# Kernel tuning notes

Hardware: AMD Instinct MI355X
Metric: run time of the kernel (lower is better)

Reference implementation:

```python
import jax, jax.numpy as jnp
import numpy as np

B, L, D, RATIO = 256, 197, 768, 8
DK = D // RATIO  # 96


def _mk_linear(key, out_f, in_f):
    kw, kb = jax.random.split(key)
    W = jax.random.normal(kw, (out_f, in_f), jnp.float32) * 0.02  # xavier_normal gain=0.02 scale
    b = jax.random.normal(kb, (out_f,), jnp.float32) * 0.02
    return W, b


def setup_inputs() -> dict:
    key = jax.random.key(0)
    ks = jax.random.split(key, 10)
    x = jax.random.normal(ks[0], (B, L, D), jnp.float32)
    y = jax.random.normal(ks[1], (B, L, D), jnp.float32)
    Wk1, bk1 = _mk_linear(ks[2], DK, D)
    Wk2, bk2 = _mk_linear(ks[3], DK, D)
    Wks, bks = _mk_linear(ks[4], DK, DK)
    Wl1, bl1 = _mk_linear(ks[5], L, L)
    Wl2, bl2 = _mk_linear(ks[6], L, L)
    Wv1, bv1 = _mk_linear(ks[7], D, D)
    Wv2, bv2 = _mk_linear(ks[8], D, D)
    # torch inits gammas to 0; use small nonzero values so outputs/grads are non-trivial
    g = jax.random.normal(ks[9], (2,), jnp.float32) * 0.1
    gamma1 = g[:1]
    gamma2 = g[1:]
    return dict(x=x, y=y, Wk1=Wk1, bk1=bk1, Wk2=Wk2, bk2=bk2, Wks=Wks, bks=bks,
                Wl1=Wl1, bl1=bl1, Wl2=Wl2, bl2=bl2, Wv1=Wv1, bv1=bv1,
                Wv2=Wv2, bv2=bv2, gamma1=gamma1, gamma2=gamma2)


def reference(x, y, Wk1, bk1, Wk2, bk2, Wks, bks, Wl1, bl1, Wl2, bl2,
              Wv1, bv1, Wv2, bv2, gamma1, gamma2):
    b, l, d = x.shape
    # shared-projected keys (B, L, DK)
    k1 = (x @ Wk1.T + bk1) @ Wks.T + bks
    k2 = (y @ Wk2.T + bk2) @ Wks.T + bks
    # faithful to torch: .view(B, -1, L) is a raw reshape (scrambles layout), then permute
    k1r = k1.reshape(b, -1, l).swapaxes(1, 2)   # (B, L, DK)
    k2r = k2.reshape(b, -1, l)                  # (B, DK, L)
    energy = jnp.einsum('blc,bcm->blm', k1r, k2r)  # (B, L, L)
    att1 = jax.nn.softmax(energy @ Wl1.T + bl1, axis=-1)                   # att_y_on_x
    att2 = jax.nn.softmax(energy.swapaxes(1, 2) @ Wl2.T + bl2, axis=-1)    # att_x_on_y
    v2 = y @ Wv2.T + bv2  # (B, L, D)
    out_y_on_x = jnp.einsum('bdl,blm->bdm', v2.swapaxes(1, 2), att1).reshape(b, l, d)
    out_x = gamma1 * out_y_on_x + x
    v1 = x @ Wv1.T + bv1
    out_x_on_y = jnp.einsum('bdl,blm->bdm', v1.swapaxes(1, 2), att2).reshape(b, l, d)
    out_y = gamma2 * out_x_on_y + y
    return (out_x, out_y)
```

## Files before the change

kernel.cpp:

```cpp
#include <hip/hip_runtime.h>
#include <math.h>

typedef unsigned short ushort;
typedef __attribute__((ext_vector_type(4))) unsigned short bfx4;
typedef __attribute__((ext_vector_type(8))) short short8;
typedef __attribute__((ext_vector_type(8))) unsigned short ushort8;
typedef __attribute__((ext_vector_type(4))) float f32x4;
typedef unsigned int u32;

#define VM_WAIT(N) asm volatile("s_waitcnt vmcnt(" #N ")" ::: "memory")
#define SBAR() asm volatile("s_barrier" ::: "memory")

__device__ __forceinline__ int swz4(int row) {
  return (row & 3) ^ ((row >> 2) & 3);
}

__device__ __forceinline__ ushort f2bf(float f) {
  u32 u = __float_as_uint(f);
  return (ushort)((u + 0x7FFF + ((u >> 16) & 1)) >> 16);
}
__device__ __forceinline__ float bf2f(ushort u) {
  u32 v = ((u32)u) << 16;
  return __uint_as_float(v);
}

__device__ __forceinline__ void gload16(const void* g, void* l) {
  __builtin_amdgcn_global_load_lds(
      (const __attribute__((address_space(1))) u32*)g,
      (__attribute__((address_space(3))) u32*)l, 16, 0, 0);
}

#define BKK 32
#define LDSP 68
__global__ __launch_bounds__(256) void gemm_generic(
    const float* __restrict__ A, const float* __restrict__ Bm, const float* __restrict__ Bm2,
    float* __restrict__ C, float* __restrict__ C2,
    int M, int N, int K, long sAi, long sAk, long sBj, long sBk, long sCi)
{
  __shared__ __align__(16) float lds_a[BKK * LDSP];
  __shared__ __align__(16) float lds_b[BKK * LDSP];
  const float* Bb = blockIdx.z ? Bm2 : Bm;
  float* Cc = blockIdx.z ? C2 : C;
  const int i0 = blockIdx.y * 64;
  const int j0 = blockIdx.x * 64;
  const int tid = threadIdx.x;
  const int tx = tid & 15, ty = tid >> 4;
  float acc[4][4] = {};
  for (int k0 = 0; k0 < K; k0 += BKK) {
    for (int idx = tid; idx < BKK * 64; idx += 256) {
      int kk = idx & (BKK - 1), ii = idx >> 5;
      int gi = i0 + ii, gk = k0 + kk;
      lds_a[kk * LDSP + ii] = (gi < M && gk < K) ? A[(long)gi * sAi + (long)gk * sAk] : 0.f;
    }
    for (int idx = tid; idx < BKK * 64; idx += 256) {
      int kk = idx & (BKK - 1), jj = idx >> 5;
      int gj = j0 + jj, gk = k0 + kk;
      lds_b[kk * LDSP + jj] = (gj < N && gk < K) ? Bb[(long)gj * sBj + (long)gk * sBk] : 0.f;
    }
    __syncthreads();
    #pragma unroll
    for (int kk = 0; kk < BKK; ++kk) {
      const float4 a4 = *reinterpret_cast<const float4*>(&lds_a[kk * LDSP + ty * 4]);
      const float4 b4 = *reinterpret_cast<const float4*>(&lds_b[kk * LDSP + tx * 4]);
      const float av[4] = {a4.x, a4.y, a4.z, a4.w};
      const float bv[4] = {b4.x, b4.y, b4.z, b4.w};
      #pragma unroll
      for (int a = 0; a < 4; ++a)
        #pragma unroll
        for (int b = 0; b < 4; ++b)
          acc[a][b] = fmaf(av[a], bv[b], acc[a][b]);
    }
    __syncthreads();
  }
  for (int a = 0; a < 4; ++a) {
    int gi = i0 + ty * 4 + a;
    if (gi >= M) continue;
    for (int b = 0; b < 4; ++b) {
      int gj = j0 + tx * 4 + b;
      if (gj >= N) continue;
      Cc[(long)gi * sCi + gj] = acc[a][b];
    }
  }
}

__global__ __launch_bounds__(256) void mfma_gemm(
    const ushort* __restrict__ A0, const ushort* __restrict__ A1,
    const ushort* __restrict__ B0, const ushort* __restrict__ B1,
    const float* __restrict__ bias0, const float* __restrict__ bias1,
    ushort* __restrict__ C0, ushort* __restrict__ C1,
    int M, int N, int K, long sAi, long sBj, long sCi)
{
  __shared__ ushort As[128 * 64];
  __shared__ ushort Bs[128 * 64];
  const int which = blockIdx.z;
  const ushort* Ab = which ? A1 : A0;
  const ushort* Bb = which ? B1 : B0;
  const float* bias = which ? bias1 : bias0;
  ushort* C = which ? C1 : C0;
  const int i0 = blockIdx.y * 128;
  const int j0 = blockIdx.x * 128;
  const int tid = threadIdx.x;
  const int wave = tid >> 6, lane = tid & 63;
  const int wm = wave >> 1, wn = wave & 1;
  const int col16 = lane & 15, krow = lane >> 4;

  f32x4 acc[4][4] = {};

  for (int k0 = 0; k0 < K; k0 += 64) {
    #pragma unroll
    for (int it = 0; it < 4; ++it) {
      int chunk = it * 256 + wave * 64 + lane;
      int row = chunk >> 3, s = chunk & 7;
      int kc = s ^ (row & 7);
      int gi = i0 + row; if (gi >= M) gi = M - 1;
      gload16(Ab + (long)gi * sAi + k0 + kc * 8, &As[chunk * 8]);
    }
    #pragma unroll
    for (int it = 0; it < 4; ++it) {
      int chunk = it * 256 + wave * 64 + lane;
      int row = chunk >> 3, s = chunk & 7;
      int kc = s ^ (row & 7);
      int gj = j0 + row; if (gj >= N) gj = N - 1;
      gload16(Bb + (long)gj * sBj + k0 + kc * 8, &Bs[chunk * 8]);
    }
    __syncthreads();
    #pragma unroll
    for (int ks = 0; ks < 2; ++ks) {
      short8 af[4], bfr[4];
      #pragma unroll
      for (int mi = 0; mi < 4; ++mi) {
        int row = wm * 64 + mi * 16 + col16;
        int slot = (ks * 4 + krow) ^ (row & 7);
        af[mi] = *(const short8*)&As[row * 64 + slot * 8];
      }
      #pragma unroll
      for (int nj = 0; nj < 4; ++nj) {
        int row = wn * 64 + nj * 16 + col16;
        int slot = (ks * 4 + krow) ^ (row & 7);
        bfr[nj] = *(const short8*)&Bs[row * 64 + slot * 8];
      }
      #pragma unroll
      for (int mi = 0; mi < 4; ++mi)
        #pragma unroll
        for (int nj = 0; nj < 4; ++nj)
          acc[mi][nj] = __builtin_amdgcn_mfma_f32_16x16x32_bf16(
              af[mi], bfr[nj], acc[mi][nj], 0, 0, 0);
    }
    __syncthreads();
  }

  const int r0 = krow * 4;
  #pragma unroll
  for (int mi = 0; mi < 4; ++mi) {
    int gi0 = i0 + wm * 64 + mi * 16 + r0;
    #pragma unroll
    for (int nj = 0; nj < 4; ++nj) {
      int gj = j0 + wn * 64 + nj * 16 + col16;
      f32x4 a = acc[mi][nj];
      #pragma unroll
      for (int r = 0; r < 4; ++r) {
        int gi = gi0 + r;
        if (gi >= M || gj >= N) continue;
        C[(long)gi * sCi + gj] = f2bf(a[r] + bias[gj]);
      }
    }
  }
}

__global__ __launch_bounds__(256) void transpose_k(
    const ushort* __restrict__ k1, const ushort* __restrict__ k2,
    ushort* __restrict__ EA1, ushort* __restrict__ EA2, int Bc)
{
  __shared__ ushort tile[32][33];
  int z = blockIdx.z;
  int which = (z >= Bc) ? 1 : 0;
  int b = which ? z - Bc : z;
  const ushort* src = (which ? k2 : k1) + (long)b * 18912;
  ushort* dst = (which ? EA2 : EA1) + (long)b * 25216;
  int l0 = blockIdx.x * 32, c0 = blockIdx.y * 32;
  int tx = threadIdx.x & 31, ty = threadIdx.x >> 5;
  for (int r = ty; r < 32; r += 8) {
    int c = c0 + r, l = l0 + tx;
    tile[r][tx] = (c < 96 && l < 197) ? src[(long)c * 197 + l] : (ushort)0;
  }
  __syncthreads();
  for (int r = ty; r < 32; r += 8) {
    int l = l0 + r, c = c0 + tx;
    if (l < 197 && c < 128) dst[(long)l * 128 + c] = tile[tx][r];
  }
}

__global__ __launch_bounds__(256) void energy_mfma(
    const ushort* __restrict__ EA1, const ushort* __restrict__ EA2,
    ushort* __restrict__ Eb, ushort* __restrict__ ETb)
{
  __shared__ ushort elds[16896];
  ushort* As = elds;
  ushort* Bs = elds + 8192;
  const int bz = blockIdx.z;
  const ushort* Ab = EA1 + 25216L * bz;
  const ushort* Bb = EA2 + 25216L * bz;
  const int i0 = blockIdx.y * 128;
  const int j0 = blockIdx.x * 128;
  const int tid = threadIdx.x;
  const int wave = tid >> 6, lane = tid & 63;
  const int wm = wave >> 1, wn = wave & 1;
  const int col16 = lane & 15, krow = lane >> 4;

  f32x4 acc[4][4] = {};

  for (int k0 = 0; k0 < 128; k0 += 64) {
    #pragma unroll
    for (int it = 0; it < 4; ++it) {
      int chunk = it * 256 + wave * 64 + lane;
      int row = chunk >> 3, s = chunk & 7;
      int kc = s ^ (row & 7);
      int gi = i0 + row; if (gi > 196) gi = 196;
      gload16(Ab + (long)gi * 128 + k0 + kc * 8, &As[chunk * 8]);
    }
    #pragma unroll
    for (int it = 0; it < 4; ++it) {
      int chunk = it * 256 + wave * 64 + lane;
      int row = chunk >> 3, s = chunk & 7;
      int kc = s ^ (row & 7);
      int gj = j0 + row; if (gj > 196) gj = 196;
      gload16(Bb + (long)gj * 128 + k0 + kc * 8, &Bs[chunk * 8]);
    }
    __syncthreads();
    #pragma unroll
    for (int ks = 0; ks < 2; ++ks) {
      short8 af[4], bfr[4];
      #pragma unroll
      for (int mi = 0; mi < 4; ++mi) {
        int row = wm * 64 + mi * 16 + col16;
        int slot = (ks * 4 + krow) ^ (row & 7);
        af[mi] = *(const short8*)&As[row * 64 + slot * 8];
      }
      #pragma unroll
      for (int nj = 0; nj < 4; ++nj) {
        int row = wn * 64 + nj * 16 + col16;
        int slot = (ks * 4 + krow) ^ (row & 7);
        bfr[nj] = *(const short8*)&Bs[row * 64 + slot * 8];
      }
      #pragma unroll
      for (int mi = 0; mi < 4; ++mi)
        #pragma unroll
        for (int nj = 0; nj < 4; ++nj)
          acc[mi][nj] = __builtin_amdgcn_mfma_f32_16x16x32_bf16(
              af[mi], bfr[nj], acc[mi][nj], 0, 0, 0);
    }
    __syncthreads();
  }

  ushort* obufT = elds;
  #pragma unroll
  for (int mi = 0; mi < 4; ++mi)
    #pragma unroll
    for (int nj = 0; nj < 4; ++nj) {
      int mcol = wn * 64 + nj * 16 + col16;
      int lrow = wm * 64 + mi * 16 + krow * 4;
      bfx4 h;
      #pragma unroll
      for (int r = 0; r < 4; ++r) h[r] = f2bf(acc[mi][nj][r]);
      *(bfx4*)&obufT[mcol * 132 + lrow] = h;
    }
  SBAR();
  {
    int lL = tid & 63, mg = tid >> 6;
    for (int it = 0; it < 32; ++it) {
      int mL = mg * 32 + it;
      int gm = j0 + mL;
      if (gm >= 197) break;
      #pragma unroll
      for (int lh = 0; lh < 2; ++lh) {
        int l = lh * 64 + lL;
        int gl = i0 + l;
        if (gl < 224)
          ETb[bz * 50432L + (long)gm * 256 + gl] =
              (gl < 197) ? obufT[mL * 132 + l] : (ushort)0;
      }
    }
  }
  {
    int mL = tid & 63, lg = tid >> 6;
    for (int it = 0; it < 32; ++it) {
      int lL = lg * 32 + it;
      int gl = i0 + lL;
      if (gl >= 197) break;
      #pragma unroll
      for (int mh = 0; mh < 2; ++mh) {
        int m = mh * 64 + mL;
        int gm = j0 + m;
        if (gm < 224)
          Eb[bz * 50432L + (long)gl * 256 + gm] =
              (gm < 197) ? obufT[m * 132 + lL] : (ushort)0;
      }
    }
  }
}

__global__ __launch_bounds__(256) void vbig_gemm(
    const ushort* __restrict__ A0, const ushort* __restrict__ A1,
    const ushort* __restrict__ B0, const ushort* __restrict__ B1,
    const float* __restrict__ bias0, const float* __restrict__ bias1,
    ushort* __restrict__ C0, ushort* __restrict__ C1,
    int ntiles, long Nc)
{
  __shared__ ushort As[2][128 * 32];
  __shared__ ushort Bs[2][128 * 32];
  const int per = 6 * ntiles;
  int bid = blockIdx.x;
  const int which = bid / per;
  bid -= which * per;
  int mtile, ntile;
  if ((ntiles & 7) == 0) {
    int xcd = bid & 7;
    int grp = bid >> 3;
    mtile = grp % 6;
    ntile = (grp / 6) * 8 + xcd;
  } else {
    ntile = bid % ntiles;
    mtile = bid / ntiles;
  }
  const ushort* Ab = (which ? A1 : A0) + (long)(mtile * 128) * 768;
  const ushort* Bb = which ? B1 : B0;
  const float* bias = which ? bias1 : bias0;
  ushort* C = which ? C1 : C0;
  const int n0 = ntile * 128;
  const int tid = threadIdx.x, wave = tid >> 6, lane = tid & 63;
  const int wm = wave >> 1, wn = wave & 1;
  const int col16 = lane & 15, kq = lane >> 4;

  f32x4 acc[4][4] = {};

  auto stage = [&](int buf, int k0) {
    const int lrow = lane >> 2, s = lane & 3;
    #pragma unroll
    for (int c0 = 0; c0 < 4; ++c0) {
      int c = wave * 4 + c0;
      if (c < 8) {
        int row = c * 16 + lrow;
        int kc = s ^ swz4(row);
        gload16(Ab + (long)row * 768 + k0 + kc * 8,
                (char*)(&As[buf][0]) + c * 1024 + lane * 16);
      } else {
        int j = (c - 8) * 16 + lrow;
        int n = n0 + j;
        int b = n / 224;
        int l = n - b * 224;
        int grow = b * 197 + (l < 197 ? l : 196);
        int kc = s ^ swz4(j);
        gload16(Bb + (long)grow * 768 + k0 + kc * 8,
                (char*)(&Bs[buf][0]) + (c - 8) * 1024 + lane * 16);
      }
    }
  };

  stage(0, 0);
  for (int t = 0; t < 24; ++t) {
    int cur = t & 1;
    if (t + 1 < 24) {
      stage(cur ^ 1, (t + 1) << 5);
      VM_WAIT(4);
    } else {
      VM_WAIT(0);
    }
    SBAR();
    short8 af[4], bfr[4];
    #pragma unroll
    for (int mi = 0; mi < 4; ++mi) {
      int arow = wm * 64 + mi * 16 + col16;
      af[mi] = *(const short8*)((const char*)(&As[cur][0]) +
                                arow * 64 + ((kq ^ swz4(arow)) << 4));
    }
    #pragma unroll
    for (int nj = 0; nj < 4; ++nj) {
      int brow = wn * 64 + nj * 16 + col16;
      bfr[nj] = *(const short8*)((const char*)(&Bs[cur][0]) +
                                 brow * 64 + ((kq ^ swz4(brow)) << 4));
    }
    #pragma unroll
    for (int mi = 0; mi < 4; ++mi)
      #pragma unroll
      for (int nj = 0; nj < 4; ++nj)
        acc[mi][nj] = __builtin_amdgcn_mfma_f32_16x16x32_bf16(
            af[mi], bfr[nj], acc[mi][nj], 0, 0, 0);
    SBAR();
  }

  #pragma unroll
  for (int mi = 0; mi < 4; ++mi) {
    #pragma unroll
    for (int r = 0; r < 4; ++r) {
      int gi = mtile * 128 + wm * 64 + mi * 16 + kq * 4 + r;
      float bv = bias[gi];
      long base = (long)gi * Nc;
      #pragma unroll
      for (int nj = 0; nj < 4; ++nj) {
        int n = n0 + wn * 64 + nj * 16 + col16;
        int b = n / 224;
        int l = n - b * 224;
        C[base + n] = (l < 197) ? f2bf(acc[mi][nj][r] + bv) : (ushort)0;
      }
    }
  }
}

__global__ __launch_bounds__(256) void att_gemm(
    const ushort* __restrict__ Wl0, const ushort* __restrict__ Wl1,
    const ushort* __restrict__ E0, const ushort* __restrict__ E1,
    const float* __restrict__ bl0, const float* __restrict__ bl1,
    ushort* __restrict__ a0, ushort* __restrict__ a1out)
{
  __shared__ ushort Aws[2][208 * 32];
  __shared__ ushort Bws[2][64 * 32];
  __shared__ float blds[208];
  const int which = blockIdx.z;
  const int bz = blockIdx.y;
  const ushort* Wl = which ? Wl1 : Wl0;
  const ushort* Bb = (which ? E1 : E0) + 50432L * bz;
  const float* bl = which ? bl1 : bl0;
  ushort* aout = which ? a1out : a0;
  const int l0 = blockIdx.x * 64;
  const int tid = threadIdx.x, wave = tid >> 6, lane = tid & 63;
  const int col16 = lane & 15, kq = lane >> 4;

  if (tid < 208) blds[tid] = (tid < 197) ? bl[tid] : 0.f;

  f32x4 acc[13] = {};

  auto stage = [&](int buf, int k0) {
    const int lrow = lane >> 2, s = lane & 3;
    #pragma unroll
    for (int c0 = 0; c0 < 5; ++c0) {
      int c = wave + c0 * 4;
      if (c >= 17) break;
      if (c < 13) {
        int row = c * 16 + lrow;
        int gr = row < 197 ? row : 196;
        int kc = s ^ swz4(row);
        gload16(Wl + (long)gr * 256 + k0 + kc * 8,
                (char*)(&Aws[buf][0]) + c * 1024 + lane * 16);
      } else {
        int row = (c - 13) * 16 + lrow;
        int gl = l0 + row; if (gl > 196) gl = 196;
        int kc = s ^ swz4(row);
        gload16(Bb + (long)gl * 256 + k0 + kc * 8,
                (char*)(&Bws[buf][0]) + (c - 13) * 1024 + lane * 16);
      }
    }
  };

  stage(0, 0);
  for (int t = 0; t < 7; ++t) {
    int cur = t & 1;
    if (t + 1 < 7) {
      stage(cur ^ 1, (t + 1) * 32);
      if (wave == 0) VM_WAIT(5); else VM_WAIT(4);
    } else {
      VM_WAIT(0);
    }
    SBAR();
    int brow = wave * 16 + col16;
    short8 bf = *(const short8*)((const char*)(&Bws[cur][0]) +
                                 brow * 64 + ((kq ^ swz4(brow)) << 4));
    #pragma unroll
    for (int j = 0; j < 13; ++j) {
      int arow = j * 16 + col16;
      short8 af = *(const short8*)((const char*)(&Aws[cur][0]) +
                                   arow * 64 + ((kq ^ swz4(arow)) << 4));
      acc[j] = __builtin_amdgcn_mfma_f32_16x16x32_bf16(af, bf, acc[j], 0, 0, 0);
    }
    SBAR();
  }

  const int c = l0 + wave * 16 + col16;
  float mx = -INFINITY;
  #pragma unroll
  for (int j = 0; j < 13; ++j)
    #pragma unroll
    for (int r = 0; r < 4; ++r) {
      int m = j * 16 + kq * 4 + r;
      float v = acc[j][r] + blds[m];
      v = (m < 197) ? v : -INFINITY;
      acc[j][r] = v;
      mx = fmaxf(mx, v);
    }
  mx = fmaxf(mx, __shfl_xor(mx, 16));
  mx = fmaxf(mx, __shfl_xor(mx, 32));
  float s = 0.f;
  #pragma unroll
  for (int j = 0; j < 13; ++j)
    #pragma unroll
    for (int r = 0; r < 4; ++r) {
      int m = j * 16 + kq * 4 + r;
      float e = (m < 197) ? __expf(acc[j][r] - mx) : 0.f;
      acc[j][r] = e;
      s += e;
    }
  s += __shfl_xor(s, 16);
  s += __shfl_xor(s, 32);
  const float inv = 1.f / s;
  ushort* ab = aout + 50432L * bz;
  #pragma unroll
  for (int j = 0; j < 13; ++j)
    #pragma unroll
    for (int r = 0; r < 4; ++r) {
      int m = j * 16 + kq * 4 + r;
      if (m < 197)
        ab[(long)m * 256 + c] = (c < 197) ? f2bf(acc[j][r] * inv) : (ushort)0;
    }
}

__global__ __launch_bounds__(512) void vout_gemm(
    const ushort* __restrict__ A0, const ushort* __restrict__ A1,
    const ushort* __restrict__ B0, const ushort* __restrict__ B1,
    const ushort* __restrict__ resid0, const ushort* __restrict__ resid1,
    const float* __restrict__ g0, const float* __restrict__ g1,
    float* __restrict__ C0, float* __restrict__ C1,
    int N, int K, long sAi, long bAs, long sBj, long bBs,
    long sCi, long bCs, int mtiles, int batches)
{
  __shared__ ushort lds_all[22528];
  const int per = mtiles * batches;
  int bid = blockIdx.x;
  const int which = bid / per;
  bid -= which * per;
  const ushort* A = which ? A1 : A0;
  const ushort* Bm = which ? B1 : B0;
  const ushort* resid = which ? resid1 : resid0;
  const float* gammaPtr = which ? g1 : g0;
  float* C = which ? C1 : C0;

  int mtile, bz;
  if ((batches & 7) == 0) {
    int xcd = bid & 7, sid = bid >> 3;
    mtile = sid % mtiles;
    bz = (sid / mtiles) * 8 + xcd;
  } else {
    mtile = bid % mtiles;
    bz = bid / mtiles;
  }
  const ushort* Ab = A + bAs * bz + (long)(mtile * 128) * sAi;
  const ushort* Bb = Bm + bBs * bz;
  const int tid = threadIdx.x, wave = tid >> 6, lane = tid & 63;
  const int wr = wave >> 1, wc = wave & 1;
  const int col16 = lane & 15, kq = lane >> 4;

  f32x4 acc[2][7] = {};

  auto stage = [&](int buf, int k0) {
    const int lrow = lane >> 2, s = lane & 3;
    #pragma unroll
    for (int c0 = 0; c0 < 3; ++c0) {
      int c = wave + c0 * 8;
      if (c >= 22) break;
      if (c < 8) {
        int row = c * 16 + lrow;
        int kc = s ^ swz4(row);
        gload16(Ab + (long)row * sAi + k0 + kc * 8,
                (char*)lds_all + buf * 8192 + c * 1024 + lane * 16);
      } else {
        int row = (c - 8) * 16 + lrow;
        int gj = row < N ? row : N - 1;
        int kc = s ^ swz4(row);
        gload16(Bb + (long)gj * sBj + k0 + kc * 8,
                (char*)lds_all + 16384 + buf * 14336 + (c - 8) * 1024 + lane * 16);
      }
    }
  };

  const int nt = K >> 5;
  stage(0, 0);
  for (int t = 0; t < nt; ++t) {
    int cur = t & 1;
    if (t + 1 < nt) {
      stage(cur ^ 1, (t + 1) << 5);
      if (wave < 6) VM_WAIT(3); else VM_WAIT(2);
    } else {
      VM_WAIT(0);
    }
    SBAR();
    short8 af[2];
    #pragma unroll
    for (int mi = 0; mi < 2; ++mi) {
      int arow = wr * 32 + mi * 16 + col16;
      af[mi] = *(const short8*)((const char*)lds_all + cur * 8192 +
                                arow * 64 + ((kq ^ swz4(arow)) << 4));
    }
    #pragma unroll
    for (int nj = 0; nj < 7; ++nj) {
      int brow = wc * 112 + nj * 16 + col16;
      short8 bf = *(const short8*)((const char*)lds_all + 16384 + cur * 14336 +
                                   brow * 64 + ((kq ^ swz4(brow)) << 4));
      #pragma unroll
      for (int mi = 0; mi < 2; ++mi)
        acc[mi][nj] = __builtin_amdgcn_mfma_f32_16x16x32_bf16(
            af[mi], bf, acc[mi][nj], 0, 0, 0);
    }
    SBAR();
  }

  const float g = gammaPtr[0];
  ushort* obufT = lds_all;
  #pragma unroll 1
  for (int c = 0; c < 2; ++c) {
    if (wc == c) {
      #pragma unroll
      for (int mi = 0; mi < 2; ++mi)
        #pragma unroll
        for (int nj = 0; nj < 7; ++nj) {
          int colL = nj * 16 + col16;
          int row = wr * 32 + mi * 16 + kq * 4;
          bfx4 h;
          #pragma unroll
          for (int r = 0; r < 4; ++r) h[r] = f2bf(g * acc[mi][nj][r]);
          *(bfx4*)&obufT[colL * 132 + row] = h;
        }
    }
    SBAR();
    {
      int colL = tid & 127, rg = tid >> 7;
      int ncols = 197 - c * 112; if (ncols > 112) ncols = 112;
      if (colL < ncols) {
        int gcol = c * 112 + colL;
        #pragma unroll 4
        for (int it = 0; it < 32; ++it) {
          int row = rg * 32 + it;
          long ci = bCs * bz + (long)(mtile * 128 + row) * 197 + gcol;
          C[ci] = bf2f(obufT[colL * 132 + row]) + bf2f(resid[ci]);
        }
      }
    }
    SBAR();
  }
}

__global__ void fuse_bias2(const float* __restrict__ Wks,
                           const float* __restrict__ bk1, const float* __restrict__ bk2,
                           const float* __restrict__ bks,
                           float* __restrict__ bf1, float* __restrict__ bf2) {
  int c = threadIdx.x;
  if (c >= 192) return;
  const float* bk = (c < 96) ? bk1 : bk2;
  float* bf = (c < 96) ? bf1 : bf2;
  int cc = (c < 96) ? c : c - 96;
  float s = bks[cc];
  for (int e = 0; e < 96; ++e) s += Wks[cc * 96 + e] * bk[e];
  bf[cc] = s;
}

__global__ __launch_bounds__(256) void conv_weights(
    const float* __restrict__ Wf1, const float* __restrict__ Wf2,
    const float* __restrict__ Wv1, const float* __restrict__ Wv2,
    const float* __restrict__ Wl1, const float* __restrict__ Wl2,
    ushort* __restrict__ Wf1b, ushort* __restrict__ Wf2b,
    ushort* __restrict__ Wv1b, ushort* __restrict__ Wv2b,
    ushort* __restrict__ Wl1b, ushort* __restrict__ Wl2b)
{
  const long total = 147456 + 1179648 + 100864;
  long stride = (long)gridDim.x * blockDim.x;
  for (long i = (long)blockIdx.x * blockDim.x + threadIdx.x; i < total; i += stride) {
    if (i < 147456) {
      long j = i;
      if (j < 73728) Wf1b[j] = f2bf(Wf1[j]);
      else Wf2b[j - 73728] = f2bf(Wf2[j - 73728]);
    } else if (i < 147456 + 1179648) {
      long j = i - 147456;
      if (j < 589824) Wv1b[j] = f2bf(Wv1[j]);
      else Wv2b[j - 589824] = f2bf(Wv2[j - 589824]);
    } else {
      long j = i - 147456 - 1179648;
      int w2 = j >= 50432;
      if (w2) j -= 50432;
      int r = (int)(j >> 8), cc = (int)(j & 255);
      const float* s = w2 ? Wl2 : Wl1;
      ushort* d = w2 ? Wl2b : Wl1b;
      d[j] = (cc < 197) ? f2bf(s[(long)r * 197 + cc]) : (ushort)0;
    }
  }
}

__global__ __launch_bounds__(256) void conv_xy(const float* __restrict__ x,
                                               const float* __restrict__ y,
                                               ushort* __restrict__ xb,
                                               ushort* __restrict__ yb, long n8) {
  long i = (long)blockIdx.x * blockDim.x + threadIdx.x;
  long stride = (long)gridDim.x * blockDim.x;
  for (; i < 2 * n8; i += stride) {
    const float* s = (i < n8) ? x : y;
    ushort* d = (i < n8) ? xb : yb;
    long j = (i < n8) ? i : i - n8;
    float4 a = ((const float4*)s)[2 * j];
    float4 b = ((const float4*)s)[2 * j + 1];
    ushort8 o;
    o[0] = f2bf(a.x); o[1] = f2bf(a.y); o[2] = f2bf(a.z); o[3] = f2bf(a.w);
    o[4] = f2bf(b.x); o[5] = f2bf(b.y); o[6] = f2bf(b.z); o[7] = f2bf(b.w);
    *(ushort8*)&d[j * 8] = o;
  }
}

extern "C" void kernel_launch(void* const* d_in, const int* in_sizes, int n_in,
                              void* d_out, int out_size, void* d_ws, size_t ws_size,
                              hipStream_t stream) {
  const float* x   = (const float*)d_in[0];
  const float* y   = (const float*)d_in[1];
  const float* Wk1 = (const float*)d_in[2];
  const float* bk1 = (const float*)d_in[3];
  const float* Wk2 = (const float*)d_in[4];
  const float* bk2 = (const float*)d_in[5];
  const float* Wks = (const float*)d_in[6];
  const float* bks = (const float*)d_in[7];
  const float* Wl1 = (const float*)d_in[8];
  const float* bl1 = (const float*)d_in[9];
  const float* Wl2 = (const float*)d_in[10];
  const float* bl2 = (const float*)d_in[11];
  const float* Wv1 = (const float*)d_in[12];
  const float* bv1 = (const float*)d_in[13];
  const float* Wv2 = (const float*)d_in[14];
  const float* bv2 = (const float*)d_in[15];
  const float* gamma1 = (const float*)d_in[16];
  const float* gamma2 = (const float*)d_in[17];
  float* out = (float*)d_out;

  const int B = 256, L = 197, D = 768;
  const long LD = (long)L * D;

  const size_t staticBytes = 3446784;
  const size_t perB = 605184 + 75648 + 100864 + 201728 + 201728 + 688128;
  int Bc = 256;
  while (Bc > 8 && staticBytes + (size_t)Bc * perB > ws_size) Bc >>= 1;

  char* p = (char*)d_ws;
  auto carve = [&](size_t bytes) { char* r = p; p += bytes; return r; };
  float*  Wf1   = (float*)carve(73728 * 4);
  float*  Wf2   = (float*)carve(73728 * 4);
  float*  bf1   = (float*)carve(512);
  float*  bf2   = (float*)carve(512);
  ushort* Wv1b  = (ushort*)carve(589824 * 2);
  ushort* Wv2b  = (ushort*)carve(589824 * 2);
  ushort* Wf1b  = (ushort*)carve(73728 * 2);
  ushort* Wf2b  = (ushort*)carve(73728 * 2);
  ushort* Wl1b  = (ushort*)carve(50432 * 2);
  ushort* Wl2b  = (ushort*)carve(50432 * 2);
  ushort* xb    = (ushort*)carve((size_t)Bc * LD * 2);
  ushort* yb    = (ushort*)carve((size_t)Bc * LD * 2);
  ushort* k1    = (ushort*)carve((size_t)Bc * 18912 * 2);
  ushort* k2    = (ushort*)carve((size_t)Bc * 18912 * 2);
  ushort* EA1   = (ushort*)carve((size_t)Bc * 25216 * 2);
  ushort* EA2   = (ushort*)carve((size_t)Bc * 25216 * 2);
  ushort* Eb    = (ushort*)carve((size_t)Bc * 50432 * 2);
  ushort* ETbuf = (ushort*)carve((size_t)Bc * 50432 * 2);
  ushort* a1    = (ushort*)carve((size_t)Bc * 50432 * 2);
  ushort* a2    = (ushort*)carve((size_t)Bc * 50432 * 2);
  const long Nc = (long)Bc * 224;
  ushort* vT    = (ushort*)carve((size_t)768 * Nc * 2);
  ushort* vT2   = (ushort*)carve((size_t)768 * Nc * 2);

  dim3 blk(256);

  gemm_generic<<<dim3(12, 2, 2), blk, 0, stream>>>(Wks, Wk1, Wk2, Wf1, Wf2,
      96, 768, 96, 96, 1, 1, 768, 768);
  fuse_bias2<<<1, 192, 0, stream>>>(Wks, bk1, bk2, bks, bf1, bf2);
  conv_weights<<<dim3(1024), blk, 0, stream>>>(Wf1, Wf2, Wv1, Wv2, Wl1, Wl2,
      Wf1b, Wf2b, Wv1b, Wv2b, Wl1b, Wl2b);

  for (int c0 = 0; c0 < B; c0 += Bc) {
    const float* xc = x + (long)c0 * LD;
    const float* yc = y + (long)c0 * LD;
    const int Mr = Bc * L;
    const int gym = (Mr + 127) / 128;

    conv_xy<<<dim3(2048), blk, 0, stream>>>(xc, yc, xb, yb, (long)Bc * LD / 8);

    mfma_gemm<<<dim3(1, gym, 2), blk, 0, stream>>>(xb, yb, Wf1b, Wf2b, bf1, bf2,
        k1, k2, Mr, 96, 768, 768, 768, 96);

    transpose_k<<<dim3(7, 4, 2 * Bc), blk, 0, stream>>>(k1, k2, EA1, EA2, Bc);

    energy_mfma<<<dim3(2, 2, Bc), blk, 0, stream>>>(EA1, EA2, Eb, ETbuf);

    att_gemm<<<dim3(4, Bc, 2), blk, 0, stream>>>(Wl1b, Wl2b, Eb, ETbuf,
        bl1, bl2, a1, a2);

    {
      int ntiles = (int)(Nc / 128);
      vbig_gemm<<<dim3(2 * 6 * ntiles), blk, 0, stream>>>(
          Wv2b, Wv1b, yb, xb, bv2, bv1, vT, vT2, ntiles, Nc);
    }

    vout_gemm<<<dim3(12 * Bc), dim3(512), 0, stream>>>(vT, vT2, a1, a2,
        xb, yb, gamma1, gamma2,
        out + (long)c0 * LD, out + (long)B * LD + (long)c0 * LD,
        197, 224, Nc, 224, 256, 50432, 197, LD, 6, Bc);
  }
}
```

Measured before the change: 662.4 us.

## Fuse value projection GEMM with attention-apply GEMM in one kernel

Replaces the separate value-projection GEMM (vbig_gemm), which wrote a bf16 vT intermediate to global memory, and the attention-apply GEMM (vout_gemm) with a single vfused_gemm. Each block computes a 64-row slice of the projected values for one batch into LDS, then multiplies that slice by the attention matrix and writes the gamma-scaled residual output. This removes the large vT round trip through HBM and one kernel launch. In exchange, tiles are smaller (64 rows instead of 128) with 256 threads and more LDS per block, which may lower MFMA efficiency and occupancy.

```diff
diff --git a/kernel.cpp b/kernel.cpp
--- a/kernel.cpp
+++ b/kernel.cpp
@@ -9,6 +9,7 @@
 typedef unsigned int u32;
 
 #define VM_WAIT(N) asm volatile("s_waitcnt vmcnt(" #N ")" ::: "memory")
+#define LGKM_WAIT() asm volatile("s_waitcnt lgkmcnt(0)" ::: "memory")
 #define SBAR() asm volatile("s_barrier" ::: "memory")
 
 __device__ __forceinline__ int swz4(int row) {
@@ -299,113 +300,6 @@
   }
 }
 
-__global__ __launch_bounds__(256) void vbig_gemm(
-    const ushort* __restrict__ A0, const ushort* __restrict__ A1,
-    const ushort* __restrict__ B0, const ushort* __restrict__ B1,
-    const float* __restrict__ bias0, const float* __restrict__ bias1,
-    ushort* __restrict__ C0, ushort* __restrict__ C1,
-    int ntiles, long Nc)
-{
-  __shared__ ushort As[2][128 * 32];
-  __shared__ ushort Bs[2][128 * 32];
-  const int per = 6 * ntiles;
-  int bid = blockIdx.x;
-  const int which = bid / per;
-  bid -= which * per;
-  int mtile, ntile;
-  if ((ntiles & 7) == 0) {
-    int xcd = bid & 7;
-    int grp = bid >> 3;
-    mtile = grp % 6;
-    ntile = (grp / 6) * 8 + xcd;
-  } else {
-    ntile = bid % ntiles;
-    mtile = bid / ntiles;
-  }
-  const ushort* Ab = (which ? A1 : A0) + (long)(mtile * 128) * 768;
-  const ushort* Bb = which ? B1 : B0;
-  const float* bias = which ? bias1 : bias0;
-  ushort* C = which ? C1 : C0;
-  const int n0 = ntile * 128;
-  const int tid = threadIdx.x, wave = tid >> 6, lane = tid & 63;
-  const int wm = wave >> 1, wn = wave & 1;
-  const int col16 = lane & 15, kq = lane >> 4;
-
-  f32x4 acc[4][4] = {};
-
-  auto stage = [&](int buf, int k0) {
-    const int lrow = lane >> 2, s = lane & 3;
-    #pragma unroll
-    for (int c0 = 0; c0 < 4; ++c0) {
-      int c = wave * 4 + c0;
-      if (c < 8) {
-        int row = c * 16 + lrow;
-        int kc = s ^ swz4(row);
-        gload16(Ab + (long)row * 768 + k0 + kc * 8,
-                (char*)(&As[buf][0]) + c * 1024 + lane * 16);
-      } else {
-        int j = (c - 8) * 16 + lrow;
-        int n = n0 + j;
-        int b = n / 224;
-        int l = n - b * 224;
-        int grow = b * 197 + (l < 197 ? l : 196);
-        int kc = s ^ swz4(j);
-        gload16(Bb + (long)grow * 768 + k0 + kc * 8,
-                (char*)(&Bs[buf][0]) + (c - 8) * 1024 + lane * 16);
-      }
-    }
-  };
-
-  stage(0, 0);
-  for (int t = 0; t < 24; ++t) {
-    int cur = t & 1;
-    if (t + 1 < 24) {
-      stage(cur ^ 1, (t + 1) << 5);
-      VM_WAIT(4);
-    } else {
-      VM_WAIT(0);
-    }
-    SBAR();
-    short8 af[4], bfr[4];
-    #pragma unroll
-    for (int mi = 0; mi < 4; ++mi) {
-      int arow = wm * 64 + mi * 16 + col16;
-      af[mi] = *(const short8*)((const char*)(&As[cur][0]) +
-                                arow * 64 + ((kq ^ swz4(arow)) << 4));
-    }
-    #pragma unroll
-    for (int nj = 0; nj < 4; ++nj) {
-      int brow = wn * 64 + nj * 16 + col16;
-      bfr[nj] = *(const short8*)((const char*)(&Bs[cur][0]) +
-                                 brow * 64 + ((kq ^ swz4(brow)) << 4));
-    }
-    #pragma unroll
-    for (int mi = 0; mi < 4; ++mi)
-      #pragma unroll
-      for (int nj = 0; nj < 4; ++nj)
-        acc[mi][nj] = __builtin_amdgcn_mfma_f32_16x16x32_bf16(
-            af[mi], bfr[nj], acc[mi][nj], 0, 0, 0);
-    SBAR();
-  }
-
-  #pragma unroll
-  for (int mi = 0; mi < 4; ++mi) {
-    #pragma unroll
-    for (int r = 0; r < 4; ++r) {
-      int gi = mtile * 128 + wm * 64 + mi * 16 + kq * 4 + r;
-      float bv = bias[gi];
-      long base = (long)gi * Nc;
-      #pragma unroll
-      for (int nj = 0; nj < 4; ++nj) {
-        int n = n0 + wn * 64 + nj * 16 + col16;
-        int b = n / 224;
-        int l = n - b * 224;
-        C[base + n] = (l < 197) ? f2bf(acc[mi][nj][r] + bv) : (ushort)0;
-      }
-    }
-  }
-}
-
 __global__ __launch_bounds__(256) void att_gemm(
     const ushort* __restrict__ Wl0, const ushort* __restrict__ Wl1,
     const ushort* __restrict__ E0, const ushort* __restrict__ E1,
@@ -512,71 +406,71 @@
     }
 }
 
-__global__ __launch_bounds__(512) void vout_gemm(
-    const ushort* __restrict__ A0, const ushort* __restrict__ A1,
-    const ushort* __restrict__ B0, const ushort* __restrict__ B1,
-    const ushort* __restrict__ resid0, const ushort* __restrict__ resid1,
+__global__ __launch_bounds__(256) void vfused_gemm(
+    const ushort* __restrict__ Wv0, const ushort* __restrict__ Wv1,
+    const ushort* __restrict__ S0, const ushort* __restrict__ S1,
+    const float* __restrict__ bv0, const float* __restrict__ bv1,
+    const ushort* __restrict__ At0, const ushort* __restrict__ At1,
+    const ushort* __restrict__ R0, const ushort* __restrict__ R1,
     const float* __restrict__ g0, const float* __restrict__ g1,
     float* __restrict__ C0, float* __restrict__ C1,
-    int N, int K, long sAi, long bAs, long sBj, long bBs,
-    long sCi, long bCs, int mtiles, int batches)
+    int Bc)
 {
-  __shared__ ushort lds_all[22528];
-  const int per = mtiles * batches;
+  __shared__ __align__(16) char lds[58368];
+  const int per = 12 * Bc;
   int bid = blockIdx.x;
   const int which = bid / per;
   bid -= which * per;
-  const ushort* A = which ? A1 : A0;
-  const ushort* Bm = which ? B1 : B0;
-  const ushort* resid = which ? resid1 : resid0;
-  const float* gammaPtr = which ? g1 : g0;
+  int dtile, b;
+  if ((Bc & 7) == 0) {
+    int xcd = bid & 7, sid = bid >> 3;
+    dtile = sid % 12;
+    b = (sid / 12) * 8 + xcd;
+  } else {
+    dtile = bid % 12;
+    b = bid / 12;
+  }
+  const ushort* Wv = (which ? Wv1 : Wv0) + (long)(dtile * 64) * 768;
+  const ushort* Sb = (which ? S1 : S0) + (long)b * 197 * 768;
+  const float* bv = which ? bv1 : bv0;
+  const ushort* attb = (which ? At1 : At0) + (long)b * 50432;
+  const ushort* resid = which ? R1 : R0;
+  const float g = (which ? g1 : g0)[0];
   float* C = which ? C1 : C0;
 
-  int mtile, bz;
-  if ((batches & 7) == 0) {
-    int xcd = bid & 7, sid = bid >> 3;
-    mtile = sid % mtiles;
-    bz = (sid / mtiles) * 8 + xcd;
-  } else {
-    mtile = bid % mtiles;
-    bz = bid / mtiles;
-  }
-  const ushort* Ab = A + bAs * bz + (long)(mtile * 128) * sAi;
-  const ushort* Bb = Bm + bBs * bz;
   const int tid = threadIdx.x, wave = tid >> 6, lane = tid & 63;
   const int wr = wave >> 1, wc = wave & 1;
   const int col16 = lane & 15, kq = lane >> 4;
 
   f32x4 acc[2][7] = {};
 
-  auto stage = [&](int buf, int k0) {
+  auto stage1 = [&](int buf, int k0) {
     const int lrow = lane >> 2, s = lane & 3;
     #pragma unroll
-    for (int c0 = 0; c0 < 3; ++c0) {
-      int c = wave + c0 * 8;
-      if (c >= 22) break;
-      if (c < 8) {
+    for (int c0 = 0; c0 < 5; ++c0) {
+      int c = wave + c0 * 4;
+      if (c >= 18) break;
+      if (c < 4) {
         int row = c * 16 + lrow;
         int kc = s ^ swz4(row);
-        gload16(Ab + (long)row * sAi + k0 + kc * 8,
-                (char*)lds_all + buf * 8192 + c * 1024 + lane * 16);
+        gload16(Wv + (long)row * 768 + k0 + kc * 8,
+                lds + buf * 4096 + c * 1024 + lane * 16);
       } else {
-        int row = (c - 8) * 16 + lrow;
-        int gj = row < N ? row : N - 1;
-        int kc = s ^ swz4(row);
-        gload16(Bb + (long)gj * sBj + k0 + kc * 8,
-                (char*)lds_all + 16384 + buf * 14336 + (c - 8) * 1024 + lane * 16);
+        int j = (c - 4) * 16 + lrow;
+        int gr = j < 197 ? j : 196;
+        int kc = s ^ swz4(j);
+        gload16(Sb + (long)gr * 768 + k0 + kc * 8,
+                lds + 8192 + buf * 14336 + (c - 4) * 1024 + lane * 16);
       }
     }
   };
 
-  const int nt = K >> 5;
-  stage(0, 0);
-  for (int t = 0; t < nt; ++t) {
+  stage1(0, 0);
+  for (int t = 0; t < 24; ++t) {
     int cur = t & 1;
-    if (t + 1 < nt) {
-      stage(cur ^ 1, (t + 1) << 5);
-      if (wave < 6) VM_WAIT(3); else VM_WAIT(2);
+    if (t + 1 < 24) {
+      stage1(cur ^ 1, (t + 1) << 5);
+      if (wave < 2) VM_WAIT(5); else VM_WAIT(4);
     } else {
       VM_WAIT(0);
     }
@@ -584,15 +478,14 @@
     short8 af[2];
     #pragma unroll
     for (int mi = 0; mi < 2; ++mi) {
-      int arow = wr * 32 + mi * 16 + col16;
-      af[mi] = *(const short8*)((const char*)lds_all + cur * 8192 +
-                                arow * 64 + ((kq ^ swz4(arow)) << 4));
+      int ar = wr * 32 + mi * 16 + col16;
+      af[mi] = *(const short8*)(lds + cur * 4096 + ar * 64 + ((kq ^ swz4(ar)) << 4));
     }
     #pragma unroll
     for (int nj = 0; nj < 7; ++nj) {
-      int brow = wc * 112 + nj * 16 + col16;
-      short8 bf = *(const short8*)((const char*)lds_all + 16384 + cur * 14336 +
-                                   brow * 64 + ((kq ^ swz4(brow)) << 4));
+      int br = wc * 112 + nj * 16 + col16;
+      short8 bf = *(const short8*)(lds + 8192 + cur * 14336 +
+                                   br * 64 + ((kq ^ swz4(br)) << 4));
       #pragma unroll
       for (int mi = 0; mi < 2; ++mi)
         acc[mi][nj] = __builtin_amdgcn_mfma_f32_16x16x32_bf16(
@@ -601,8 +494,73 @@
     SBAR();
   }
 
-  const float g = gammaPtr[0];
-  ushort* obufT = lds_all;
+  ushort* vlds = (ushort*)(lds + 28672);
+  #pragma unroll
+  for (int mi = 0; mi < 2; ++mi)
+    #pragma unroll
+    for (int r = 0; r < 4; ++r) {
+      int dl = wr * 32 + mi * 16 + kq * 4 + r;
+      float bvv = bv[dtile * 64 + dl];
+      #pragma unroll
+      for (int nj = 0; nj < 7; ++nj) {
+        int l = wc * 112 + nj * 16 + col16;
+        vlds[dl * 232 + l] = f2bf(acc[mi][nj][r] + bvv);
+      }
+    }
+  LGKM_WAIT();
+  SBAR();
+
+  #pragma unroll
+  for (int mi = 0; mi < 2; ++mi)
+    #pragma unroll
+    for (int nj = 0; nj < 7; ++nj)
+      acc[mi][nj] = (f32x4){0.f, 0.f, 0.f, 0.f};
+
+  auto stage2 = [&](int buf, int k0) {
+    const int lrow = lane >> 2, s = lane & 3;
+    #pragma unroll
+    for (int c0 = 0; c0 < 4; ++c0) {
+      int c = wave + c0 * 4;
+      if (c >= 14) break;
+      int m = c * 16 + lrow;
+      int gm = m < 197 ? m : 196;
+      int kc = s ^ swz4(m);
+      gload16(attb + (long)gm * 256 + k0 + kc * 8,
+              lds + buf * 14336 + c * 1024 + lane * 16);
+    }
+  };
+
+  stage2(0, 0);
+  for (int t = 0; t < 7; ++t) {
+    int cur = t & 1;
+    if (t + 1 < 7) {
+      stage2(cur ^ 1, (t + 1) << 5);
+      if (wave < 2) VM_WAIT(4); else VM_WAIT(3);
+    } else {
+      VM_WAIT(0);
+    }
+    SBAR();
+    const int k0 = t << 5;
+    short8 af[2];
+    #pragma unroll
+    for (int mi = 0; mi < 2; ++mi) {
+      int ar = wr * 32 + mi * 16 + col16;
+      af[mi] = *(const short8*)((const char*)vlds + ar * 464 + k0 * 2 + kq * 16);
+    }
+    #pragma unroll
+    for (int nj = 0; nj < 7; ++nj) {
+      int br = wc * 112 + nj * 16 + col16;
+      short8 bf = *(const short8*)(lds + cur * 14336 +
+                                   br * 64 + ((kq ^ swz4(br)) << 4));
+      #pragma unroll
+      for (int mi = 0; mi < 2; ++mi)
+        acc[mi][nj] = __builtin_amdgcn_mfma_f32_16x16x32_bf16(
+            af[mi], bf, acc[mi][nj], 0, 0, 0);
+    }
+    SBAR();
+  }
+
+  ushort* obufT = (ushort*)lds;
   #pragma unroll 1
   for (int c = 0; c < 2; ++c) {
     if (wc == c) {
@@ -615,7 +573,7 @@
           bfx4 h;
           #pragma unroll
           for (int r = 0; r < 4; ++r) h[r] = f2bf(g * acc[mi][nj][r]);
-          *(bfx4*)&obufT[colL * 132 + row] = h;
+          *(bfx4*)&obufT[colL * 68 + row] = h;
         }
     }
     SBAR();
@@ -627,8 +585,8 @@
         #pragma unroll 4
         for (int it = 0; it < 32; ++it) {
           int row = rg * 32 + it;
-          long ci = bCs * bz + (long)(mtile * 128 + row) * 197 + gcol;
-          C[ci] = bf2f(obufT[colL * 132 + row]) + bf2f(resid[ci]);
+          long ci = (long)b * 151296 + (long)(dtile * 64 + row) * 197 + gcol;
+          C[ci] = bf2f(obufT[colL * 68 + row]) + bf2f(resid[ci]);
         }
       }
     }
@@ -727,7 +685,7 @@
   const long LD = (long)L * D;
 
   const size_t staticBytes = 3446784;
-  const size_t perB = 605184 + 75648 + 100864 + 201728 + 201728 + 688128;
+  const size_t perB = 605184 + 75648 + 100864 + 201728 + 201728;
   int Bc = 256;
   while (Bc > 8 && staticBytes + (size_t)Bc * perB > ws_size) Bc >>= 1;
 
@@ -753,9 +711,6 @@
   ushort* ETbuf = (ushort*)carve((size_t)Bc * 50432 * 2);
   ushort* a1    = (ushort*)carve((size_t)Bc * 50432 * 2);
   ushort* a2    = (ushort*)carve((size_t)Bc * 50432 * 2);
-  const long Nc = (long)Bc * 224;
-  ushort* vT    = (ushort*)carve((size_t)768 * Nc * 2);
-  ushort* vT2   = (ushort*)carve((size_t)768 * Nc * 2);
 
   dim3 blk(256);
 
@@ -783,15 +738,8 @@
     att_gemm<<<dim3(4, Bc, 2), blk, 0, stream>>>(Wl1b, Wl2b, Eb, ETbuf,
         bl1, bl2, a1, a2);
 
-    {
-      int ntiles = (int)(Nc / 128);
-      vbig_gemm<<<dim3(2 * 6 * ntiles), blk, 0, stream>>>(
-          Wv2b, Wv1b, yb, xb, bv2, bv1, vT, vT2, ntiles, Nc);
-    }
-
-    vout_gemm<<<dim3(12 * Bc), dim3(512), 0, stream>>>(vT, vT2, a1, a2,
-        xb, yb, gamma1, gamma2,
-        out + (long)c0 * LD, out + (long)B * LD + (long)c0 * LD,
-        197, 224, Nc, 224, 256, 50432, 197, LD, 6, Bc);
-  }
-}
+    vfused_gemm<<<dim3(2 * 12 * Bc), blk, 0, stream>>>(
+        Wv2b, Wv1b, yb, xb, bv2, bv1, a1, a2, xb, yb, gamma1, gamma2,
+        out + (long)c0 * LD, out + (long)B * LD + (long)c0 * LD, Bc);
+  }
+}
```

After: 636.7 us. -3.9%, faster.
